# Optimization experiments

Hardware: AMD Instinct MI355X
Metric: run time of the kernel (lower is better)

## Reference

```python
import jax, jax.numpy as jnp
import numpy as np

USER_NUM = 128          # K: users, also equals RIS elements N due to W_v packing
NOISE_DBM = -80.0       # downlink_noise_power
N0 = 10.0 ** (NOISE_DBM / 10.0) / 1000.0  # = exp(p/10*ln10)/1000


def setup_inputs() -> dict:
    key = jax.random.key(0)
    k1, k2, k3, k4, k5 = jax.random.split(key, 5)
    M, K, N = 1024, USER_NUM, USER_NUM  # antennas, users, RIS elements
    return {
        "W_v": jax.random.normal(k1, (M + 1, 2 * K), dtype=jnp.float32),
        "A_real": jax.random.normal(k2, (K, M, N), dtype=jnp.float32),
        "A_imag": jax.random.normal(k3, (K, M, N), dtype=jnp.float32),
        "h_d_real": jax.random.normal(k4, (K, M), dtype=jnp.float32),
        "h_d_imag": jax.random.normal(k5, (K, M), dtype=jnp.float32),
    }


def reference(W_v, A_real, A_imag, h_d_real, h_d_imag):
    # unpack: row 0 is v (RIS phase vector), rows 1.. are W (beamformers)
    v = W_v[0]            # [2N]
    W = W_v[1:]           # [M, 2K]
    C = W.shape[1] // 2   # = K = user_num = N
    W_re, W_im = W[:, :C], W[:, C:]      # [M, K]
    v_re, v_im = v[:C], v[C:]            # [N]

    # effective channel h_k = h_d[k] + A[k] @ v  (complex product, real arithmetic)
    Av_re = jnp.einsum('kmn,n->km', A_real, v_re) - jnp.einsum('kmn,n->km', A_imag, v_im)
    Av_im = jnp.einsum('kmn,n->km', A_imag, v_re) + jnp.einsum('kmn,n->km', A_real, v_im)
    h_re = h_d_real + Av_re              # [K, M]
    h_im = h_d_imag + Av_im              # [K, M]

    # gamma[k, i] = w_i^T h_k (complex, no conjugate, matching the block-matrix math)
    g_re = h_re @ W_re - h_im @ W_im     # [K, K]
    g_im = h_re @ W_im + h_im @ W_re     # [K, K]
    mag = jnp.sqrt(g_re * g_re + g_im * g_im)  # |gamma| (modulus, NOT squared)

    sig = jnp.diagonal(mag)                       # |w_k^T h_k|
    interf = jnp.sum(mag, axis=1) - sig           # sum_{i != k} |w_i^T h_k|
    R = sig / (interf + N0)                       # per-user 'rate' term
    return (-jnp.sum(R) * 1.0e6)[None]            # shape (1,), matches torch.zeros(1) accumulator
```

## Files before the change

kernel.cpp:

```cpp
#include <hip/hip_runtime.h>


#define KM_ROWS (128 * 1024)

__global__ __launch_bounds__(256) void compute_h_kernel(
    const float* __restrict__ A_real,
    const float* __restrict__ A_imag,
    const float* __restrict__ W_v,
    const float* __restrict__ h_d_real,
    const float* __restrict__ h_d_imag,
    float* __restrict__ h_re,
    float* __restrict__ h_im)
{
    const int lane = threadIdx.x & 63;
    const int wave = threadIdx.x >> 6;
    const int subl = lane & 31;
    const int row  = (blockIdx.x * 4 + wave) * 2 + (lane >> 5);

    const float4 ar = ((const float4*)(A_real + (size_t)row * 128))[subl];
    const float4 ai = ((const float4*)(A_imag + (size_t)row * 128))[subl];
    const float4 vr = ((const float4*)W_v)[subl];
    const float4 vi = ((const float4*)W_v)[32 + subl];

    float p_re = ar.x*vr.x + ar.y*vr.y + ar.z*vr.z + ar.w*vr.w
               - (ai.x*vi.x + ai.y*vi.y + ai.z*vi.z + ai.w*vi.w);
    float p_im = ai.x*vr.x + ai.y*vr.y + ai.z*vr.z + ai.w*vr.w
               + ar.x*vi.x + ar.y*vi.y + ar.z*vi.z + ar.w*vi.w;

    #pragma unroll
    for (int off = 1; off < 32; off <<= 1) {
        p_re += __shfl_xor(p_re, off);
        p_im += __shfl_xor(p_im, off);
    }
    if (subl == 0) {
        h_re[row] = h_d_real[row] + p_re;
        h_im[row] = h_d_imag[row] + p_im;
    }
}

__global__ __launch_bounds__(256) void gemm_rate_kernel(
    const float* __restrict__ h_re,
    const float* __restrict__ h_im,
    const float* __restrict__ W_v,
    float* __restrict__ out)
{
    const int k = blockIdx.x;
    const int t = threadIdx.x;
    const int c = t & 127;
    const int half = t >> 7;

    __shared__ float sh_re[1024];
    __shared__ float sh_im[1024];
    ((float4*)sh_re)[t] = ((const float4*)(h_re + (size_t)k * 1024))[t];
    ((float4*)sh_im)[t] = ((const float4*)(h_im + (size_t)k * 1024))[t];
    __syncthreads();

    float gre = 0.f, gim = 0.f;
    const float* Wbase = W_v + 256;
    const int m0 = half * 512;
    #pragma unroll 8
    for (int m = m0; m < m0 + 512; ++m) {
        float wr = Wbase[m * 256 + c];
        float wi = Wbase[m * 256 + 128 + c];
        float hr = sh_re[m];
        float hi = sh_im[m];
        gre = fmaf(hr, wr, gre);
        gre = fmaf(-hi, wi, gre);
        gim = fmaf(hr, wi, gim);
        gim = fmaf(hi, wr, gim);
    }

    __shared__ float s_re[256], s_im[256];
    s_re[t] = gre; s_im[t] = gim;
    __syncthreads();

    __shared__ float s_wsum[2];
    __shared__ float s_sig;
    float mag = 0.f;
    if (t < 128) {
        float gr = s_re[t] + s_re[t + 128];
        float gi = s_im[t] + s_im[t + 128];
        mag = sqrtf(gr * gr + gi * gi);
        if (t == k) s_sig = mag;
    }
    float v = mag;
    #pragma unroll
    for (int off = 32; off > 0; off >>= 1) v += __shfl_xor(v, off);
    if ((t & 63) == 0 && t < 128) s_wsum[t >> 6] = v;
    __syncthreads();

    if (t == 0) {
        float total  = s_wsum[0] + s_wsum[1];
        float sig    = s_sig;
        float interf = total - sig;
        float R      = sig / (interf + 1e-11f);
        atomicAdd(out, -R * 1e6f);
    }
}

extern "C" void kernel_launch(void* const* d_in, const int* in_sizes, int n_in,
                              void* d_out, int out_size, void* d_ws, size_t ws_size,
                              hipStream_t stream) {
    const float* W_v      = (const float*)d_in[0];
    const float* A_real   = (const float*)d_in[1];
    const float* A_imag   = (const float*)d_in[2];
    const float* h_d_real = (const float*)d_in[3];
    const float* h_d_imag = (const float*)d_in[4];
    float* out  = (float*)d_out;
    float* h_re = (float*)d_ws;
    float* h_im = h_re + KM_ROWS;

    hipMemsetAsync(d_out, 0, sizeof(float), stream);

    compute_h_kernel<<<16384, 256, 0, stream>>>(A_real, A_imag, W_v,
                                                h_d_real, h_d_imag, h_re, h_im);
    gemm_rate_kernel<<<128, 256, 0, stream>>>(h_re, h_im, W_v, out);
}
```

Measured before the change: 190.6 us.

## Grid-stride compute_h and split-M GEMM into partial and rate kernels

compute_h now has each 16-lane group handle one row using two float4 loads per matrix, and runs a grid-stride loop over a smaller grid so the v loads are hoisted out of the loop. The 128-block GEMM, which underfills the GPU, is split along M into 8 slices (1024 blocks) that write partial sums to workspace. A new rate kernel reduces those partials and computes the rate. The aim is more bandwidth in the A streaming pass and more parallelism in the GEMM, at the cost of an extra kernel launch and extra workspace traffic.

```diff
diff --git a/kernel.cpp b/kernel.cpp
--- a/kernel.cpp
+++ b/kernel.cpp
@@ -2,6 +2,10 @@
 
 
 #define KM_ROWS (128 * 1024)
+
+__device__ __forceinline__ float dot4(float4 a, float4 b) {
+    return a.x*b.x + a.y*b.y + a.z*b.z + a.w*b.w;
+}
 
 __global__ __launch_bounds__(256) void compute_h_kernel(
     const float* __restrict__ A_real,
@@ -13,55 +17,67 @@
     float* __restrict__ h_im)
 {
     const int lane = threadIdx.x & 63;
-    const int wave = threadIdx.x >> 6;
-    const int subl = lane & 31;
-    const int row  = (blockIdx.x * 4 + wave) * 2 + (lane >> 5);
+    const int sub  = lane & 15;
+    const int rsub = lane >> 4;
+    const int wid  = blockIdx.x * 4 + (threadIdx.x >> 6);
+    const int nw   = gridDim.x * 4;
 
-    const float4 ar = ((const float4*)(A_real + (size_t)row * 128))[subl];
-    const float4 ai = ((const float4*)(A_imag + (size_t)row * 128))[subl];
-    const float4 vr = ((const float4*)W_v)[subl];
-    const float4 vi = ((const float4*)W_v)[32 + subl];
+    const float4 vr0 = ((const float4*)W_v)[sub];
+    const float4 vr1 = ((const float4*)W_v)[sub + 16];
+    const float4 vi0 = ((const float4*)W_v)[32 + sub];
+    const float4 vi1 = ((const float4*)W_v)[48 + sub];
 
-    float p_re = ar.x*vr.x + ar.y*vr.y + ar.z*vr.z + ar.w*vr.w
-               - (ai.x*vi.x + ai.y*vi.y + ai.z*vi.z + ai.w*vi.w);
-    float p_im = ai.x*vr.x + ai.y*vr.y + ai.z*vr.z + ai.w*vr.w
-               + ar.x*vi.x + ar.y*vi.y + ar.z*vi.z + ar.w*vi.w;
+    for (int base = wid; base < KM_ROWS / 4; base += nw) {
+        const int row = base * 4 + rsub;
+        const float4* Ar = (const float4*)(A_real + (size_t)row * 128);
+        const float4* Ai = (const float4*)(A_imag + (size_t)row * 128);
+        const float4 a0 = Ar[sub];
+        const float4 a1 = Ar[sub + 16];
+        const float4 b0 = Ai[sub];
+        const float4 b1 = Ai[sub + 16];
 
-    #pragma unroll
-    for (int off = 1; off < 32; off <<= 1) {
-        p_re += __shfl_xor(p_re, off);
-        p_im += __shfl_xor(p_im, off);
-    }
-    if (subl == 0) {
-        h_re[row] = h_d_real[row] + p_re;
-        h_im[row] = h_d_imag[row] + p_im;
+        float p_re = dot4(a0, vr0) + dot4(a1, vr1) - dot4(b0, vi0) - dot4(b1, vi1);
+        float p_im = dot4(b0, vr0) + dot4(b1, vr1) + dot4(a0, vi0) + dot4(a1, vi1);
+
+        #pragma unroll
+        for (int off = 1; off < 16; off <<= 1) {
+            p_re += __shfl_xor(p_re, off);
+            p_im += __shfl_xor(p_im, off);
+        }
+        if (sub == 0) {
+            h_re[row] = h_d_real[row] + p_re;
+            h_im[row] = h_d_imag[row] + p_im;
+        }
     }
 }
 
-__global__ __launch_bounds__(256) void gemm_rate_kernel(
+__global__ __launch_bounds__(256) void gemm_partial_kernel(
     const float* __restrict__ h_re,
     const float* __restrict__ h_im,
     const float* __restrict__ W_v,
-    float* __restrict__ out)
+    float* __restrict__ part_re,
+    float* __restrict__ part_im)
 {
-    const int k = blockIdx.x;
+    const int k     = blockIdx.x >> 3;
+    const int slice = blockIdx.x & 7;
     const int t = threadIdx.x;
     const int c = t & 127;
     const int half = t >> 7;
 
-    __shared__ float sh_re[1024];
-    __shared__ float sh_im[1024];
-    ((float4*)sh_re)[t] = ((const float4*)(h_re + (size_t)k * 1024))[t];
-    ((float4*)sh_im)[t] = ((const float4*)(h_im + (size_t)k * 1024))[t];
+    __shared__ float sh_re[128], sh_im[128];
+    if (t < 128) {
+        sh_re[t] = h_re[k * 1024 + slice * 128 + t];
+        sh_im[t] = h_im[k * 1024 + slice * 128 + t];
+    }
     __syncthreads();
 
+    const float* Wb = W_v + 256 + (size_t)(slice * 128) * 256;
     float gre = 0.f, gim = 0.f;
-    const float* Wbase = W_v + 256;
-    const int m0 = half * 512;
+    const int m0 = half * 64;
     #pragma unroll 8
-    for (int m = m0; m < m0 + 512; ++m) {
-        float wr = Wbase[m * 256 + c];
-        float wi = Wbase[m * 256 + 128 + c];
+    for (int m = m0; m < m0 + 64; ++m) {
+        float wr = Wb[m * 256 + c];
+        float wi = Wb[m * 256 + 128 + c];
         float hr = sh_re[m];
         float hi = sh_im[m];
         gre = fmaf(hr, wr, gre);
@@ -73,27 +89,43 @@
     __shared__ float s_re[256], s_im[256];
     s_re[t] = gre; s_im[t] = gim;
     __syncthreads();
+    if (t < 128) {
+        const int idx = (slice * 128 + k) * 128 + t;
+        part_re[idx] = s_re[t] + s_re[t + 128];
+        part_im[idx] = s_im[t] + s_im[t + 128];
+    }
+}
 
-    __shared__ float s_wsum[2];
+__global__ __launch_bounds__(128) void rate_kernel(
+    const float* __restrict__ part_re,
+    const float* __restrict__ part_im,
+    float* __restrict__ out)
+{
+    const int k = blockIdx.x;
+    const int c = threadIdx.x;
+
+    float gr = 0.f, gi = 0.f;
+    #pragma unroll
+    for (int s = 0; s < 8; ++s) {
+        gr += part_re[(s * 128 + k) * 128 + c];
+        gi += part_im[(s * 128 + k) * 128 + c];
+    }
+    float mag = sqrtf(gr * gr + gi * gi);
+
     __shared__ float s_sig;
-    float mag = 0.f;
-    if (t < 128) {
-        float gr = s_re[t] + s_re[t + 128];
-        float gi = s_im[t] + s_im[t + 128];
-        mag = sqrtf(gr * gr + gi * gi);
-        if (t == k) s_sig = mag;
-    }
+    __shared__ float s_w[2];
+    if (c == k) s_sig = mag;
+
     float v = mag;
     #pragma unroll
     for (int off = 32; off > 0; off >>= 1) v += __shfl_xor(v, off);
-    if ((t & 63) == 0 && t < 128) s_wsum[t >> 6] = v;
+    if ((c & 63) == 0) s_w[c >> 6] = v;
     __syncthreads();
 
-    if (t == 0) {
-        float total  = s_wsum[0] + s_wsum[1];
-        float sig    = s_sig;
-        float interf = total - sig;
-        float R      = sig / (interf + 1e-11f);
+    if (c == 0) {
+        float total  = s_w[0] + s_w[1];
+        float interf = total - s_sig;
+        float R      = s_sig / (interf + 1e-11f);
         atomicAdd(out, -R * 1e6f);
     }
 }
@@ -107,12 +139,16 @@
     const float* h_d_real = (const float*)d_in[3];
     const float* h_d_imag = (const float*)d_in[4];
     float* out  = (float*)d_out;
-    float* h_re = (float*)d_ws;
-    float* h_im = h_re + KM_ROWS;
+
+    float* h_re    = (float*)d_ws;
+    float* h_im    = h_re + KM_ROWS;
+    float* part_re = h_im + KM_ROWS;
+    float* part_im = part_re + 8 * 128 * 128;
 
     hipMemsetAsync(d_out, 0, sizeof(float), stream);
 
-    compute_h_kernel<<<16384, 256, 0, stream>>>(A_real, A_imag, W_v,
-                                                h_d_real, h_d_imag, h_re, h_im);
-    gemm_rate_kernel<<<128, 256, 0, stream>>>(h_re, h_im, W_v, out);
+    compute_h_kernel<<<2048, 256, 0, stream>>>(A_real, A_imag, W_v,
+                                               h_d_real, h_d_imag, h_re, h_im);
+    gemm_partial_kernel<<<1024, 256, 0, stream>>>(h_re, h_im, W_v, part_re, part_im);
+    rate_kernel<<<128, 128, 0, stream>>>(part_re, part_im, out);
 }
```

New measurement: 166.8 us. 1.14x faster.
